# Optimization experiments

Hardware: AMD Instinct MI355X
Metric: run time of the kernel (lower is better)

## Reference

```python
import jax, jax.numpy as jnp
import numpy as np

BOUNDS = [0.01, 1.0, 100.0]
STEPS = [128, 128]
ALPHA_C = 0.01          # cfg.renderer.alpha
N_IMPORTANCE = 128      # cfg.renderer.importance_steps
N_RAYS = 65536


def _zvals_log_coarse():
    # matches torch.linspace(log10(b[i]), log10(b[i+1]) - seg/steps[i], steps[i]) per segment
    segs = []
    for i, s in enumerate(STEPS):
        lo = np.log10(BOUNDS[i]); hi = np.log10(BOUNDS[i + 1])
        segs.append(np.linspace(lo, hi - (hi - lo) / s, s, dtype=np.float32))
    return np.concatenate(segs)


def _seg_scale():
    tot = float(sum(STEPS))
    return np.concatenate([np.full(s, s / tot, dtype=np.float32) for s in STEPS])


def setup_inputs() -> dict:
    key = jax.random.key(0)
    k1, k2, k3, k4 = jax.random.split(key, 4)
    sigmas_coarse = jax.random.uniform(k1, (N_RAYS, sum(STEPS)), dtype=jnp.float32) * 5.0
    sigmas_fine = jax.random.uniform(k2, (N_RAYS, N_IMPORTANCE), dtype=jnp.float32) * 5.0
    rgbs_fine = jax.random.uniform(k3, (N_RAYS, N_IMPORTANCE, 3), dtype=jnp.float32)
    bg_color = jax.random.uniform(k4, (3,), dtype=jnp.float32)
    return {"sigmas_coarse": sigmas_coarse, "sigmas_fine": sigmas_fine,
            "rgbs_fine": rgbs_fine, "bg_color": bg_color}


def _weights_from_sigmas(sigmas, z_log):
    # delta[:, :-1] = diff(z_log), last delta = 0 (as in efficient_sampling)
    delta = jnp.concatenate([z_log[:, 1:] - z_log[:, :-1], jnp.zeros_like(z_log[:, :1])], -1)
    alpha = 1.0 - jnp.exp(-sigmas * delta)
    alpha_shift = jnp.concatenate([jnp.zeros_like(alpha[:, :1]), alpha[:, :-1]], -1)
    trans = jnp.cumprod(1.0 - alpha_shift, axis=-1)   # transmittance
    return alpha * trans


def _reweight(weights):
    # pad with zeros, 3-tap max blur, floor by alpha/S, per-segment rescale, normalize
    wpad = jnp.pad(weights, ((0, 0), (1, 1)))
    w = 0.5 * (jnp.maximum(wpad[:, :-2], wpad[:, 1:-1]) + jnp.maximum(wpad[:, 1:-1], wpad[:, 2:]))
    w = w + ALPHA_C / w.shape[-1]
    w = w * jnp.asarray(_seg_scale())
    return w / jnp.sum(w, axis=-1, keepdims=True)


def _sample_pdf(bins, weights, n_samples):
    # weights already normalized -> pdf; deterministic stratified u for reproducibility
    cdf = jnp.cumsum(weights, axis=-1)                     # [N, S]
    u = (jnp.arange(n_samples, dtype=bins.dtype) + 0.5) / n_samples
    u = jnp.broadcast_to(u, (bins.shape[0], n_samples))    # [N, n]
    inds = jax.vmap(lambda c, uu: jnp.searchsorted(c, uu, side='right'))(cdf, u)
    S = bins.shape[-1]
    below = jnp.clip(inds - 1, 0, S - 1)
    above = jnp.clip(inds, 0, S - 1)
    cdf_b = jnp.take_along_axis(cdf, below, -1)
    cdf_a = jnp.take_along_axis(cdf, above, -1)
    bin_b = jnp.take_along_axis(bins, below, -1)
    bin_a = jnp.take_along_axis(bins, above, -1)
    denom = jnp.where(cdf_a - cdf_b < 1e-5, 1.0, cdf_a - cdf_b)
    t = (u - cdf_b) / denom
    return bin_b + t * (bin_a - bin_b)


def reference(sigmas_coarse, sigmas_fine, rgbs_fine, bg_color):
    # --- efficient_sampling (no_grad path) ---
    z_log = jnp.broadcast_to(jnp.asarray(_zvals_log_coarse()), sigmas_coarse.shape)
    w_coarse = _weights_from_sigmas(sigmas_coarse, z_log)
    w_re = _reweight(w_coarse)
    z_log_fine = _sample_pdf(z_log, w_re, N_IMPORTANCE)     # [N, n_imp], sorted
    z_fine = jnp.power(10.0, z_log_fine)
    # --- render_rays_log-style compositing on fine samples ---
    w_fine = _weights_from_sigmas(sigmas_fine, z_log_fine)
    image = jnp.einsum('ns,nsc->nc', w_fine, rgbs_fine)
    image = image + (1.0 - jnp.sum(w_fine, -1)[..., None]) * bg_color
    invdepth = jnp.sum(w_fine / z_fine, axis=-1)
    lo = np.float32(np.log10(BOUNDS[0])); hi = np.float32(np.log10(BOUNDS[-1]))
    z_log_s = (z_log_fine - lo) / (hi - lo)
    return image, invdepth, w_fine, z_log_s
```

## Files before the change

### kernel.cpp

```cpp
#include <hip/hip_runtime.h>

#define SC 256
#define NF 128

template<int CTRL, int RM, int BM>
__device__ __forceinline__ float dpp_add(float x) {
    int s = __builtin_amdgcn_update_dpp(0, __float_as_int(x), CTRL, RM, BM, true);
    return x + __int_as_float(s);
}
template<int CTRL, int RM, int BM>
__device__ __forceinline__ int dpp_imax(int x) {
    int s = __builtin_amdgcn_update_dpp(0, x, CTRL, RM, BM, true);
    return (x > s) ? x : s;
}
template<int CTRL>
__device__ __forceinline__ float dpp_mov0(float x) {
    return __int_as_float(__builtin_amdgcn_update_dpp(0, __float_as_int(x), CTRL, 0xF, 0xF, true));
}
__device__ __forceinline__ float lane_f(float x, int l) {
    return __int_as_float(__builtin_amdgcn_readlane(__float_as_int(x), l));
}

__device__ __forceinline__ float wave_incl_scan(float x) {
    x = dpp_add<0x111, 0xF, 0xF>(x);
    x = dpp_add<0x112, 0xF, 0xF>(x);
    x = dpp_add<0x114, 0xF, 0xF>(x);
    x = dpp_add<0x118, 0xF, 0xF>(x);
    x = dpp_add<0x142, 0xA, 0xF>(x);
    x = dpp_add<0x143, 0xC, 0xF>(x);
    return x;
}

__device__ __forceinline__ int wave_incl_scan_imax(int x) {
    x = dpp_imax<0x111, 0xF, 0xF>(x);
    x = dpp_imax<0x112, 0xF, 0xF>(x);
    x = dpp_imax<0x114, 0xF, 0xF>(x);
    x = dpp_imax<0x118, 0xF, 0xF>(x);
    x = dpp_imax<0x142, 0xA, 0xF>(x);
    x = dpp_imax<0x143, 0xC, 0xF>(x);
    return x;
}

__device__ __forceinline__ float wave_sum_lane0(float x) {
    x = dpp_add<0xB1, 0xF, 0xF>(x);
    x = dpp_add<0x4E, 0xF, 0xF>(x);
    x = dpp_add<0x124, 0xF, 0xF>(x);
    x = dpp_add<0x128, 0xF, 0xF>(x);
    return x + lane_f(x, 16) + lane_f(x, 32) + lane_f(x, 48);
}

__device__ __forceinline__ int bin_klo(float c) {
    int k = (int)ceilf(fmaf(128.0f, c, -0.5f));
    return (k < 0) ? 0 : k;
}

struct Ray {
    float4 sc4;
    float2 sf;
    float2 ra, rb, rc;
};

__device__ __forceinline__ Ray load_ray(const float* __restrict__ sig_c,
                                        const float* __restrict__ sig_f,
                                        const float* __restrict__ rgb_f,
                                        int ray, int lane) {
    Ray d;
    d.sc4 = *reinterpret_cast<const float4*>(sig_c + (size_t)ray * SC + 4 * lane);
    d.sf  = *reinterpret_cast<const float2*>(sig_f + (size_t)ray * NF + 2 * lane);
    const float2* rp = reinterpret_cast<const float2*>(rgb_f + (size_t)ray * (NF * 3) + 6 * lane);
    d.ra = rp[0]; d.rb = rp[1]; d.rc = rp[2];
    return d;
}

__device__ __forceinline__ void compute_ray(
    const Ray& rd, int ray, int lane,
    float* __restrict__ cdf, int* __restrict__ idx,
    float bg0, float bg1, float bg2,
    float* __restrict__ out, int n_rays)
{
    const float DLT = 0.015625f;
    float x0 = rd.sc4.x * DLT;
    float x1 = rd.sc4.y * DLT;
    float x2 = rd.sc4.z * DLT;
    float x3 = (lane == 63) ? 0.0f : rd.sc4.w * DLT;

    float p0 = x0, p1 = p0 + x1, p2 = p1 + x2, p3 = p2 + x3;
    float incl = wave_incl_scan(p3);
    float excl = incl - p3;

    float T0 = __expf(-excl);
    float T1 = __expf(-(excl + p0));
    float T2 = __expf(-(excl + p1));
    float T3 = __expf(-(excl + p2));
    float T4 = __expf(-(excl + p3));
    float w0 = T0 - T1, w1 = T1 - T2, w2 = T2 - T3, w3 = T3 - T4;

    float wl = dpp_mov0<0x138>(w3);
    float wr = dpp_mov0<0x130>(w0);

    const float FLOOR = 0.01f / 256.0f;
    float m01 = fmaxf(w0, w1), m12 = fmaxf(w1, w2), m23 = fmaxf(w2, w3);
    float r0 = 0.5f * (fmaxf(wl, w0) + m01) + FLOOR;
    float r1 = 0.5f * (m01 + m12) + FLOOR;
    float r2 = 0.5f * (m12 + m23) + FLOOR;
    float r3 = 0.5f * (m23 + fmaxf(w3, wr)) + FLOOR;

    float q0 = r0, q1 = q0 + r1, q2 = q1 + r2, q3 = q2 + r3;
    float incl2 = wave_incl_scan(q3);
    float excl2 = incl2 - q3;
    float total = lane_f(incl2, 63);
    float inv_total = __builtin_amdgcn_rcpf(total);

    float c0 = (excl2 + q0) * inv_total;
    float c1 = (excl2 + q1) * inv_total;
    float c2 = (excl2 + q2) * inv_total;
    float c3 = (excl2 + q3) * inv_total;
    float cprev = dpp_mov0<0x138>(c3);

    *reinterpret_cast<float4*>(&cdf[4 * lane]) = make_float4(c0, c1, c2, c3);

    *reinterpret_cast<int2*>(&idx[2 * lane]) = make_int2(-1, -1);

    const int jb = 4 * lane;
    int k0 = bin_klo(cprev);
    int k1 = bin_klo(c0);
    int k2 = bin_klo(c1);
    int k3 = bin_klo(c2);
    int k4 = bin_klo(c3);
    if (k0 < k1 && k0 < NF) idx[k0] = jb + 0;
    if (k1 < k2 && k1 < NF) idx[k1] = jb + 1;
    if (k2 < k3 && k2 < NF) idx[k2] = jb + 2;
    if (k3 < k4 && k3 < NF) idx[k3] = jb + 3;

    __asm__ __volatile__("" ::: "memory");

    const int2 jraw = *reinterpret_cast<const int2*>(&idx[2 * lane]);
    int m  = (jraw.x > jraw.y) ? jraw.x : jraw.y;
    int M  = wave_incl_scan_imax(m);
    int E  = __builtin_amdgcn_update_dpp(0, M, 0x138, 0xF, 0xF, true);
    int j0 = (E  > jraw.x) ? E  : jraw.x;
    int j1 = (j0 > jraw.y) ? j0 : jraw.y;

    int b0 = (j0 > 0) ? j0 - 1 : 0;
    int b1 = (j1 > 0) ? j1 - 1 : 0;
    float ca0 = cdf[j0], cb0 = cdf[b0];
    float ca1 = cdf[j1], cb1 = cdf[b1];

    const float u0 = ((float)(2 * lane) + 0.5f) * 0.0078125f;
    const float u1 = ((float)(2 * lane) + 1.5f) * 0.0078125f;

    float dn0 = ca0 - cb0;  dn0 = (dn0 < 1e-5f) ? 1.0f : dn0;
    float dn1 = ca1 - cb1;  dn1 = (dn1 < 1e-5f) ? 1.0f : dn1;
    float sc0f = (j0 > 0) ? DLT : 0.0f;
    float sc1f = (j1 > 0) ? DLT : 0.0f;
    float zL0 = fmaf((float)b0, DLT, -2.0f);
    float zL1 = fmaf((float)b1, DLT, -2.0f);
    float zl0 = fmaf((u0 - cb0) * __builtin_amdgcn_rcpf(dn0), sc0f, zL0);
    float zl1 = fmaf((u1 - cb1) * __builtin_amdgcn_rcpf(dn1), sc1f, zL1);

    float znext = dpp_mov0<0x130>(zl0);
    float d0 = zl1 - zl0;
    float d1 = (lane == 63) ? 0.0f : (znext - zl1);

    float y0 = rd.sf.x * d0;
    float y1 = rd.sf.y * d1;
    float ps = y0 + y1;
    float fincl = wave_incl_scan(ps);
    float fexcl = fincl - ps;

    float U0 = __expf(-fexcl);
    float U1 = __expf(-(fexcl + y0));
    float U2 = __expf(-(fexcl + ps));
    float wf0 = U0 - U1, wf1 = U1 - U2;

    float img_r = wf0 * rd.ra.x + wf1 * rd.rb.y;
    float img_g = wf0 * rd.ra.y + wf1 * rd.rc.x;
    float img_b = wf0 * rd.rb.x + wf1 * rd.rc.y;
    float wsum  = wf0 + wf1;
    float invd = wf0 * __exp10f(-zl0) + wf1 * __exp10f(-zl1);

    img_r = wave_sum_lane0(img_r);
    img_g = wave_sum_lane0(img_g);
    img_b = wave_sum_lane0(img_b);
    wsum  = wave_sum_lane0(wsum);
    invd  = wave_sum_lane0(invd);

    float* out_img  = out;
    float* out_invd = out + (size_t)n_rays * 3;
    float* out_wf   = out + (size_t)n_rays * 4;
    float* out_zs   = out + (size_t)n_rays * 4 + (size_t)n_rays * NF;

    if (lane == 0) {
        float one_m = 1.0f - wsum;
        out_img[(size_t)ray * 3 + 0] = img_r + one_m * bg0;
        out_img[(size_t)ray * 3 + 1] = img_g + one_m * bg1;
        out_img[(size_t)ray * 3 + 2] = img_b + one_m * bg2;
        out_invd[ray] = invd;
    }
    *reinterpret_cast<float2*>(out_wf + (size_t)ray * NF + 2 * lane) =
        make_float2(wf0, wf1);
    *reinterpret_cast<float2*>(out_zs + (size_t)ray * NF + 2 * lane) =
        make_float2((zl0 + 2.0f) * 0.25f, (zl1 + 2.0f) * 0.25f);
}

__global__ __launch_bounds__(256) void nerf_render_kernel(
    const float* __restrict__ sig_c,
    const float* __restrict__ sig_f,
    const float* __restrict__ rgb_f,
    const float* __restrict__ bg,
    float* __restrict__ out,
    int n_rays)
{
    const int lane = threadIdx.x & 63;
    const int wid  = threadIdx.x >> 6;

    __shared__ float s_cdf[4][SC];
    __shared__ int   s_idx[4][NF];
    float* cdf = s_cdf[wid];
    int*   idx = s_idx[wid];

    const int n_waves = (int)(gridDim.x << 2);
    const int w       = (int)(blockIdx.x << 2) + wid;
    const int rpw     = (n_rays + n_waves - 1) / n_waves;
    const int r_base  = w * rpw;
    if (r_base >= n_rays) return;

    const float bg0 = bg[0], bg1 = bg[1], bg2 = bg[2];

    const int last = n_rays - 1;
    Ray A = load_ray(sig_c, sig_f, rgb_f, r_base <= last ? r_base : last, lane);
    Ray B;
    for (int i = 0; i < rpw; i += 2) {
        int rA = r_base + i;
        int rB = r_base + i + 1;
        int rC = r_base + i + 2;
        B = load_ray(sig_c, sig_f, rgb_f, rB <= last ? rB : last, lane);
        if (rA <= last) compute_ray(A, rA, lane, cdf, idx, bg0, bg1, bg2, out, n_rays);
        A = load_ray(sig_c, sig_f, rgb_f, rC <= last ? rC : last, lane);
        if (rB <= last) compute_ray(B, rB, lane, cdf, idx, bg0, bg1, bg2, out, n_rays);
    }
}

extern "C" void kernel_launch(void* const* d_in, const int* in_sizes, int n_in,
                              void* d_out, int out_size, void* d_ws, size_t ws_size,
                              hipStream_t stream) {
    const float* sig_c = (const float*)d_in[0];
    const float* sig_f = (const float*)d_in[1];
    const float* rgb_f = (const float*)d_in[2];
    const float* bg    = (const float*)d_in[3];
    float* out = (float*)d_out;

    const int n_rays = in_sizes[1] / NF;
    int blocks_needed = (n_rays + 3) / 4;
    int blocks = blocks_needed < 2048 ? blocks_needed : 2048;
    dim3 grid(blocks), block(256);
    hipLaunchKernelGGL(nerf_render_kernel, grid, block, 0, stream,
                       sig_c, sig_f, rgb_f, bg, out, n_rays);
}
```

Before: 246.4 us.

## Replace persistent ray loop with two rays per wave and interleaved phases

Drops the persistent grid of 2048 blocks in which each wave looped over many rays with software prefetch. Each wave now handles exactly two rays and launches enough blocks to cover all of them, splitting the per-ray work into three phases that are interleaved across the two rays to hide LDS and dependency latency. This trades the explicit load-ahead pipelining for more resident waves, relying on occupancy to hide memory latency. Shared memory per block doubles, which may lower occupancy, and block launch overhead grows.

```diff
diff --git a/kernel.cpp b/kernel.cpp
--- a/kernel.cpp
+++ b/kernel.cpp
@@ -72,12 +72,9 @@
     return d;
 }
 
-__device__ __forceinline__ void compute_ray(
-    const Ray& rd, int ray, int lane,
-    float* __restrict__ cdf, int* __restrict__ idx,
-    float bg0, float bg1, float bg2,
-    float* __restrict__ out, int n_rays)
-{
+__device__ __forceinline__ void phase1(const Ray& rd, int lane,
+                                       float* __restrict__ cdf,
+                                       int* __restrict__ idx) {
     const float DLT = 0.015625f;
     float x0 = rd.sc4.x * DLT;
     float x1 = rd.sc4.y * DLT;
@@ -118,7 +115,6 @@
     float cprev = dpp_mov0<0x138>(c3);
 
     *reinterpret_cast<float4*>(&cdf[4 * lane]) = make_float4(c0, c1, c2, c3);
-
     *reinterpret_cast<int2*>(&idx[2 * lane]) = make_int2(-1, -1);
 
     const int jb = 4 * lane;
@@ -131,9 +127,12 @@
     if (k1 < k2 && k1 < NF) idx[k1] = jb + 1;
     if (k2 < k3 && k2 < NF) idx[k2] = jb + 2;
     if (k3 < k4 && k3 < NF) idx[k3] = jb + 3;
-
-    __asm__ __volatile__("" ::: "memory");
-
+}
+
+__device__ __forceinline__ float2 phase2(int lane,
+                                         const float* __restrict__ cdf,
+                                         const int* __restrict__ idx) {
+    const float DLT = 0.015625f;
     const int2 jraw = *reinterpret_cast<const int2*>(&idx[2 * lane]);
     int m  = (jraw.x > jraw.y) ? jraw.x : jraw.y;
     int M  = wave_incl_scan_imax(m);
@@ -157,7 +156,13 @@
     float zL1 = fmaf((float)b1, DLT, -2.0f);
     float zl0 = fmaf((u0 - cb0) * __builtin_amdgcn_rcpf(dn0), sc0f, zL0);
     float zl1 = fmaf((u1 - cb1) * __builtin_amdgcn_rcpf(dn1), sc1f, zL1);
-
+    return make_float2(zl0, zl1);
+}
+
+__device__ __forceinline__ void phase3(const Ray& rd, float zl0, float zl1,
+                                       int ray, int lane,
+                                       float bg0, float bg1, float bg2,
+                                       float* __restrict__ out, int n_rays) {
     float znext = dpp_mov0<0x130>(zl0);
     float d0 = zl1 - zl0;
     float d1 = (lane == 63) ? 0.0f : (znext - zl1);
@@ -214,31 +219,33 @@
     const int lane = threadIdx.x & 63;
     const int wid  = threadIdx.x >> 6;
 
-    __shared__ float s_cdf[4][SC];
-    __shared__ int   s_idx[4][NF];
-    float* cdf = s_cdf[wid];
-    int*   idx = s_idx[wid];
-
-    const int n_waves = (int)(gridDim.x << 2);
-    const int w       = (int)(blockIdx.x << 2) + wid;
-    const int rpw     = (n_rays + n_waves - 1) / n_waves;
-    const int r_base  = w * rpw;
-    if (r_base >= n_rays) return;
-
+    __shared__ float s_cdf[8][SC];
+    __shared__ int   s_idx[8][NF];
+
+    const int w  = (int)(blockIdx.x << 2) + wid;
+    const int rA = 2 * w;
+    const int rB = 2 * w + 1;
+    if (rA >= n_rays) return;
+    const int last = n_rays - 1;
+
+    Ray A = load_ray(sig_c, sig_f, rgb_f, rA, lane);
+    Ray B = load_ray(sig_c, sig_f, rgb_f, rB <= last ? rB : last, lane);
     const float bg0 = bg[0], bg1 = bg[1], bg2 = bg[2];
 
-    const int last = n_rays - 1;
-    Ray A = load_ray(sig_c, sig_f, rgb_f, r_base <= last ? r_base : last, lane);
-    Ray B;
-    for (int i = 0; i < rpw; i += 2) {
-        int rA = r_base + i;
-        int rB = r_base + i + 1;
-        int rC = r_base + i + 2;
-        B = load_ray(sig_c, sig_f, rgb_f, rB <= last ? rB : last, lane);
-        if (rA <= last) compute_ray(A, rA, lane, cdf, idx, bg0, bg1, bg2, out, n_rays);
-        A = load_ray(sig_c, sig_f, rgb_f, rC <= last ? rC : last, lane);
-        if (rB <= last) compute_ray(B, rB, lane, cdf, idx, bg0, bg1, bg2, out, n_rays);
-    }
+    float* cdfA = s_cdf[2 * wid + 0];  int* idxA = s_idx[2 * wid + 0];
+    float* cdfB = s_cdf[2 * wid + 1];  int* idxB = s_idx[2 * wid + 1];
+
+    phase1(A, lane, cdfA, idxA);
+    phase1(B, lane, cdfB, idxB);
+
+    __asm__ __volatile__("" ::: "memory");
+
+    float2 zA = phase2(lane, cdfA, idxA);
+    float2 zB = phase2(lane, cdfB, idxB);
+
+    phase3(A, zA.x, zA.y, rA, lane, bg0, bg1, bg2, out, n_rays);
+    if (rB <= last)
+        phase3(B, zB.x, zB.y, rB, lane, bg0, bg1, bg2, out, n_rays);
 }
 
 extern "C" void kernel_launch(void* const* d_in, const int* in_sizes, int n_in,
@@ -251,9 +258,8 @@
     float* out = (float*)d_out;
 
     const int n_rays = in_sizes[1] / NF;
-    int blocks_needed = (n_rays + 3) / 4;
-    int blocks = blocks_needed < 2048 ? blocks_needed : 2048;
-    dim3 grid(blocks), block(256);
+    const int n_waves = (n_rays + 1) / 2;
+    dim3 grid((n_waves + 3) / 4), block(256);
     hipLaunchKernelGGL(nerf_render_kernel, grid, block, 0, stream,
                        sig_c, sig_f, rgb_f, bg, out, n_rays);
 }
```

Measured after the change: 238.4 us. 3.2% less time.
